# Kernel tuning notes

Measured on AMD Instinct MI355X. Metric: run time of the kernel, lower is better.

Reference implementation:

```python
import jax, jax.numpy as jnp
import numpy as np

N = 20000
E_RAND = 320000
NEG_SLOPE = 0.2


def setup_inputs() -> dict:
    key = jax.random.key(0)
    ks = jax.random.split(key, 10)
    x = jax.random.normal(ks[0], (N, 768), dtype=jnp.float32)
    src = jax.random.randint(ks[1], (E_RAND,), 0, N)
    dst = jax.random.randint(ks[2], (E_RAND,), 0, N)
    loop = jnp.arange(N)
    edge_index = jnp.stack([jnp.concatenate([src, loop]),
                            jnp.concatenate([dst, loop])])  # [2, 340000]
    s = 1.0 / np.sqrt(768.0)
    W1 = jax.random.normal(ks[3], (768, 768), dtype=jnp.float32) * s
    a_src1 = jax.random.normal(ks[4], (8, 96), dtype=jnp.float32) * 0.1
    a_dst1 = jax.random.normal(ks[5], (8, 96), dtype=jnp.float32) * 0.1
    b1 = jnp.zeros((768,), dtype=jnp.float32)
    W2 = jax.random.normal(ks[6], (768, 768), dtype=jnp.float32) * s
    a_src2 = jax.random.normal(ks[7], (1, 768), dtype=jnp.float32) * 0.1
    a_dst2 = jax.random.normal(ks[8], (1, 768), dtype=jnp.float32) * 0.1
    b2 = jnp.zeros((768,), dtype=jnp.float32)
    return {"x": x, "edge_index": edge_index, "W1": W1, "a_src1": a_src1,
            "a_dst1": a_dst1, "b1": b1, "W2": W2, "a_src2": a_src2,
            "a_dst2": a_dst2, "b2": b2}


def gat_layer(x, W, a_src, a_dst, bias, src, dst, heads, out_c, concat):
    n = x.shape[0]
    h = (x @ W).reshape(n, heads, out_c)                      # [N,H,C]
    al_s = jnp.einsum('nhc,hc->nh', h, a_src)                 # [N,H]
    al_d = jnp.einsum('nhc,hc->nh', h, a_dst)
    e = jax.nn.leaky_relu(al_s[src] + al_d[dst], NEG_SLOPE)   # [E,H]
    m = jax.ops.segment_max(e, dst, num_segments=n)           # segment softmax
    ex = jnp.exp(e - m[dst])
    z = jax.ops.segment_sum(ex, dst, num_segments=n)
    alpha = ex / (z[dst] + 1e-16)                             # [E,H]
    msg = h[src] * alpha[:, :, None]                          # [E,H,C]
    out = jax.ops.segment_sum(msg, dst, num_segments=n)       # [N,H,C]
    out = out.reshape(n, heads * out_c) if concat else out.mean(axis=1)
    return out + bias


def reference(x, edge_index, W1, a_src1, a_dst1, b1, W2, a_src2, a_dst2, b2):
    src, dst = edge_index[0], edge_index[1]
    h = gat_layer(x, W1, a_src1, a_dst1, b1, src, dst, heads=8, out_c=96, concat=True)
    h = jax.nn.elu(h)
    out = gat_layer(h, W2, a_src2, a_dst2, b2, src, dst, heads=1, out_c=768, concat=False)
    return out
```

## Files before the change

### kernel.cpp

```cpp
#include <hip/hip_runtime.h>
#include <cstdint>
#include <cstddef>

typedef _Float16 f16;
typedef _Float16 f16x4 __attribute__((ext_vector_type(4)));
typedef _Float16 f16x8 __attribute__((ext_vector_type(8)));
typedef float f32x4 __attribute__((ext_vector_type(4)));

#define LRELU_SLOPE 0.2f

#define GLL16(g, l)                                                          \
  __builtin_amdgcn_global_load_lds(                                          \
      (const __attribute__((address_space(1))) void*)(g),                    \
      (__attribute__((address_space(3))) void*)(l), 16, 0, 0)

__global__ __launch_bounds__(256) void k_prep_xh(const float* __restrict__ x,
                                                 f16* __restrict__ xh,
                                                 int nvalid, int npad) {
  int total = npad * 192;
  for (int idx = blockIdx.x * blockDim.x + threadIdx.x; idx < total;
       idx += gridDim.x * blockDim.x) {
    int row = idx / 192;
    f16x4 o;
    if (row < nvalid) {
      const float4 v = *(const float4*)(x + (size_t)idx * 4);
      o[0] = (f16)v.x; o[1] = (f16)v.y; o[2] = (f16)v.z; o[3] = (f16)v.w;
    } else {
      o[0] = (f16)0.f; o[1] = (f16)0.f; o[2] = (f16)0.f; o[3] = (f16)0.f;
    }
    *(f16x4*)(xh + (size_t)idx * 4) = o;
  }
}

__global__ __launch_bounds__(256) void k_transpose_w2(const float* __restrict__ W1,
                                                      const float* __restrict__ W2,
                                                      f16* __restrict__ Wt1,
                                                      f16* __restrict__ Wt2) {
  const float* W = blockIdx.z ? W2 : W1;
  f16* Wt = blockIdx.z ? Wt2 : Wt1;
  __shared__ float tile[32][33];
  int bn = blockIdx.x * 32;
  int bk = blockIdx.y * 32;
  int tx = threadIdx.x & 31, ty = threadIdx.x >> 5;
  #pragma unroll
  for (int r = ty; r < 32; r += 8)
    tile[r][tx] = W[(size_t)(bk + r) * 768 + bn + tx];
  __syncthreads();
  #pragma unroll
  for (int r = ty; r < 32; r += 8)
    Wt[(size_t)(bn + r) * 768 + bk + tx] = (f16)tile[tx][r];
}

__global__ void k_hist(const int* __restrict__ dst, int E, int* __restrict__ counts) {
  for (int e = blockIdx.x * blockDim.x + threadIdx.x; e < E;
       e += gridDim.x * blockDim.x) atomicAdd(&counts[dst[e]], 1);
}

__global__ __launch_bounds__(1024) void k_scan_block(const int* __restrict__ counts,
                                                     int* __restrict__ starts,
                                                     int* __restrict__ cursor, int n) {
  const int t = threadIdx.x;
  const int nthr = 1024;
  const int chunk = (n + nthr - 1) / nthr;
  const int base = t * chunk;
  int tsum = 0;
  for (int i = 0; i < chunk; i++) {
    int idx = base + i;
    if (idx < n) tsum += counts[idx];
  }
  int lane = t & 63, wv = t >> 6;
  int s = tsum;
  #pragma unroll
  for (int off = 1; off < 64; off <<= 1) {
    int tmp = __shfl_up(s, off);
    if (lane >= off) s += tmp;
  }
  __shared__ int wsum[16];
  if (lane == 63) wsum[wv] = s;
  __syncthreads();
  int woff = 0;
  for (int w = 0; w < wv; w++) woff += wsum[w];
  int run = woff + s - tsum;
  for (int i = 0; i < chunk; i++) {
    int idx = base + i;
    if (idx < n) {
      starts[idx] = run;
      cursor[idx] = run;
      run += counts[idx];
    }
  }
  if (t == nthr - 1) starts[n] = run;
}

__global__ void k_fill(const int* __restrict__ src, const int* __restrict__ dst, int E,
                       int* __restrict__ cursor, int* __restrict__ src_sorted) {
  for (int e = blockIdx.x * blockDim.x + threadIdx.x; e < E;
       e += gridDim.x * blockDim.x) {
    int slot = atomicAdd(&cursor[dst[e]], 1);
    src_sorted[slot] = src[e];
  }
}

__global__ __launch_bounds__(256) void k_gemm_f16(const f16* __restrict__ A,
                                                  const f16* __restrict__ Bt,
                                                  f16* __restrict__ C, int Mvalid) {
  __shared__ __align__(16) f16 As[2][8192];
  __shared__ __align__(16) f16 Bs[2][8192];
  const int K = 768;
  const int tid = threadIdx.x;

  const int nwg = gridDim.x;
  const int orig = blockIdx.x;
  const int q = nwg >> 3, r = nwg & 7;
  const int xcd = orig & 7;
  const int wgid = (xcd < r ? xcd * (q + 1) : r * (q + 1) + (xcd - r) * q) + (orig >> 3);
  const int bm = (wgid / 6) * 128;
  const int bn = (wgid - (wgid / 6) * 6) * 128;

  const int lane = tid & 63;
  const int wave = tid >> 6;
  const int wr = (wave >> 1) * 64;
  const int wc = (wave & 1) * 64;

  size_t goffA[4], goffB[4];
  #pragma unroll
  for (int p = 0; p < 4; p++) {
    const int cell = p * 256 + tid;
    const int row = cell >> 3;
    const int cl = (cell & 7) ^ (row & 7);
    goffA[p] = (size_t)(bm + row) * K + cl * 8;
    goffB[p] = (size_t)(bn + row) * K + cl * 8;
  }

  f32x4 acc[4][4];
  const f32x4 vzero = {0.f, 0.f, 0.f, 0.f};
  #pragma unroll
  for (int i = 0; i < 4; i++)
    #pragma unroll
    for (int j = 0; j < 4; j++) acc[i][j] = vzero;

  const int fr = lane & 15;
  const int fq = lane >> 4;

  #define STAGE(buf, k0)                                                      \
    do {                                                                      \
      _Pragma("unroll")                                                       \
      for (int p = 0; p < 4; p++) {                                           \
        GLL16(A + goffA[p] + (k0), &As[buf][p * 2048 + wave * 512]);          \
        GLL16(Bt + goffB[p] + (k0), &Bs[buf][p * 2048 + wave * 512]);         \
      }                                                                       \
    } while (0)

  STAGE(0, 0);
  asm volatile("s_waitcnt vmcnt(0)" ::: "memory");
  __builtin_amdgcn_s_barrier();

  const int NT = K / 64;
  int cur = 0;
  for (int t = 0; t < NT; t++) {
    if (t + 1 < NT) STAGE(cur ^ 1, (t + 1) * 64);
    #pragma unroll
    for (int ks = 0; ks < 2; ks++) {
      f16x8 af[4], bf[4];
      #pragma unroll
      for (int i = 0; i < 4; i++) {
        const int rr = wr + i * 16 + fr;
        const int phys = (ks * 4 + fq) ^ (rr & 7);
        af[i] = *(const f16x8*)(&As[cur][rr * 64 + phys * 8]);
      }
      #pragma unroll
      for (int j = 0; j < 4; j++) {
        const int rr = wc + j * 16 + fr;
        const int phys = (ks * 4 + fq) ^ (rr & 7);
        bf[j] = *(const f16x8*)(&Bs[cur][rr * 64 + phys * 8]);
      }
      #pragma unroll
      for (int i = 0; i < 4; i++)
        #pragma unroll
        for (int j = 0; j < 4; j++)
          acc[i][j] = __builtin_amdgcn_mfma_f32_16x16x32_f16(af[i], bf[j], acc[i][j], 0, 0, 0);
    }
    asm volatile("s_waitcnt vmcnt(0)" ::: "memory");
    __builtin_amdgcn_s_barrier();
    cur ^= 1;
  }
  #undef STAGE

  #pragma unroll
  for (int i = 0; i < 4; i++) {
    #pragma unroll
    for (int j = 0; j < 4; j++) {
      const int col = bn + wc + j * 16 + fr;
      #pragma unroll
      for (int rg = 0; rg < 4; rg++) {
        const int row = bm + wr + i * 16 + fq * 4 + rg;
        if (row < Mvalid) C[(size_t)row * 768 + col] = (f16)acc[i][j][rg];
      }
    }
  }
}

template <int H>
__global__ __launch_bounds__(256) void k_al(const f16* __restrict__ h,
                                            const float* __restrict__ a_src,
                                            const float* __restrict__ a_dst,
                                            float* __restrict__ als,
                                            float* __restrict__ ald, int N) {
  int node = blockIdx.x * 4 + (threadIdx.x >> 6);
  int lane = threadIdx.x & 63;
  if (node >= N) return;
  const f16x4* hp = (const f16x4*)(h + (size_t)node * 768 + lane * 12);
  float ss = 0.f, sd = 0.f;
  int cbase = lane * 12;
  #pragma unroll
  for (int q = 0; q < 3; q++) {
    f16x4 hv = hp[q];
    #pragma unroll
    for (int j = 0; j < 4; j++) {
      int c = cbase + q * 4 + j;
      float v = (float)hv[j];
      ss += v * a_src[c];
      sd += v * a_dst[c];
    }
  }
  const int red = (H == 8) ? 8 : 64;
  #pragma unroll
  for (int off = 1; off < red; off <<= 1) {
    ss += __shfl_xor(ss, off);
    sd += __shfl_xor(sd, off);
  }
  if (H == 8) {
    if ((lane & 7) == 0) {
      als[(size_t)node * 8 + (lane >> 3)] = ss;
      ald[(size_t)node * 8 + (lane >> 3)] = sd;
    }
  } else {
    if (lane == 0) { als[node] = ss; ald[node] = sd; }
  }
}

template <int H, bool FINAL>
__global__ __launch_bounds__(192) void k_aggregate(
    const f16* __restrict__ h, const float* __restrict__ als,
    const float* __restrict__ ald, const int* __restrict__ starts,
    const int* __restrict__ src_sorted, const float* __restrict__ bias,
    void* __restrict__ outv, int nvalid) {
  const int n = blockIdx.x;
  const int t = threadIdx.x;
  if (n >= nvalid) return;
  __shared__ float s_ex[256 * H];
  __shared__ int s_src[256];
  __shared__ float s_zp[3][H];
  const int start = starts[n];
  const int deg = starts[n + 1] - start;
  const int lane = t & 63, wv = t >> 6;
  const int hA = (H == 8) ? (t & 7) : 0;
  const int myh = (H == 8) ? (t / 24) : 0;
  const float ald_A = ald[(size_t)n * H + hA];

  float zpart = 0.f;
  float4 acc = {0.f, 0.f, 0.f, 0.f};

  for (int cb = 0; cb < deg; cb += 256) {
    const int cnt = min(256, deg - cb);
    for (int idx = t; idx < cnt * H; idx += 192) {
      const int e = (H == 8) ? (idx >> 3) : idx;
      const int s = src_sorted[start + cb + e];
      if (H == 1 || (idx & 7) == 0) s_src[e] = s;
      float v = als[(size_t)s * H + hA] + ald_A;
      v = v > 0.f ? v : LRELU_SLOPE * v;
      const float ex = __expf(v);
      s_ex[idx] = ex;
      zpart += ex;
    }
    __syncthreads();
    for (int e = 0; e < cnt; e++) {
      const f16x4 hv = *(const f16x4*)(h + (size_t)s_src[e] * 768 + 4 * t);
      const float a = s_ex[e * H + myh];
      acc.x += a * (float)hv[0];
      acc.y += a * (float)hv[1];
      acc.z += a * (float)hv[2];
      acc.w += a * (float)hv[3];
    }
    __syncthreads();
  }

  if (H == 8) {
    #pragma unroll
    for (int off = 8; off < 64; off <<= 1) zpart += __shfl_xor(zpart, off);
    if (lane < 8) s_zp[wv][lane] = zpart;
  } else {
    #pragma unroll
    for (int off = 1; off < 64; off <<= 1) zpart += __shfl_xor(zpart, off);
    if (lane == 0) s_zp[wv][0] = zpart;
  }
  __syncthreads();
  const float z = s_zp[0][myh] + s_zp[1][myh] + s_zp[2][myh];
  const float inv = 1.f / (z + 1e-16f);

  const float4 bv = *(const float4*)(bias + 4 * t);
  float v0 = acc.x * inv + bv.x;
  float v1 = acc.y * inv + bv.y;
  float v2 = acc.z * inv + bv.z;
  float v3 = acc.w * inv + bv.w;
  if (!FINAL) {
    v0 = v0 > 0.f ? v0 : expm1f(v0);
    v1 = v1 > 0.f ? v1 : expm1f(v1);
    v2 = v2 > 0.f ? v2 : expm1f(v2);
    v3 = v3 > 0.f ? v3 : expm1f(v3);
    f16x4 o;
    o[0] = (f16)v0; o[1] = (f16)v1; o[2] = (f16)v2; o[3] = (f16)v3;
    *(f16x4*)((f16*)outv + (size_t)n * 768 + 4 * t) = o;
  } else {
    float4 o = {v0, v1, v2, v3};
    *(float4*)((float*)outv + (size_t)n * 768 + 4 * t) = o;
  }
}

extern "C" void kernel_launch(void* const* d_in, const int* in_sizes, int n_in,
                              void* d_out, int out_size, void* d_ws, size_t ws_size,
                              hipStream_t stream) {
  const float* x   = (const float*)d_in[0];
  const int*   ei  = (const int*)d_in[1];
  const float* W1  = (const float*)d_in[2];
  const float* as1 = (const float*)d_in[3];
  const float* ad1 = (const float*)d_in[4];
  const float* b1  = (const float*)d_in[5];
  const float* W2  = (const float*)d_in[6];
  const float* as2 = (const float*)d_in[7];
  const float* ad2 = (const float*)d_in[8];
  const float* b2  = (const float*)d_in[9];

  const int N = in_sizes[0] / 768;
  const int E = in_sizes[1] / 2;
  const int Mpad = (N + 127) & ~127;
  const int* srcp = ei;
  const int* dstp = ei + E;

  char* p = (char*)d_ws;
  auto alloc = [&](size_t b) { char* r = p; p += (b + 255) & ~(size_t)255; return r; };
  f16*   bufX   = (f16*)alloc((size_t)Mpad * 768 * sizeof(f16));
  f16*   bufH   = (f16*)alloc((size_t)Mpad * 768 * sizeof(f16));
  f16*   Wt1    = (f16*)alloc((size_t)768 * 768 * sizeof(f16));
  f16*   Wt2    = (f16*)alloc((size_t)768 * 768 * sizeof(f16));
  float* als1   = (float*)alloc((size_t)N * 8 * sizeof(float));
  float* ald1   = (float*)alloc((size_t)N * 8 * sizeof(float));
  float* als2   = (float*)alloc((size_t)N * sizeof(float));
  float* ald2   = (float*)alloc((size_t)N * sizeof(float));
  int*   counts = (int*)alloc((size_t)N * sizeof(int));
  int*   starts = (int*)alloc(((size_t)N + 1) * sizeof(int));
  int*   cursor = (int*)alloc((size_t)N * sizeof(int));
  int*   srcs   = (int*)alloc((size_t)E * sizeof(int));

  hipMemsetAsync(counts, 0, (size_t)N * sizeof(int), stream);
  k_hist<<<dim3(512), dim3(256), 0, stream>>>(dstp, E, counts);
  k_scan_block<<<dim3(1), dim3(1024), 0, stream>>>(counts, starts, cursor, N);
  k_fill<<<dim3(512), dim3(256), 0, stream>>>(srcp, dstp, E, cursor, srcs);

  k_prep_xh<<<dim3(1024), dim3(256), 0, stream>>>(x, bufX, N, Mpad);
  k_transpose_w2<<<dim3(24, 24, 2), dim3(256), 0, stream>>>(W1, W2, Wt1, Wt2);

  const int nwg = (Mpad / 128) * 6;

  k_gemm_f16<<<dim3(nwg), dim3(256), 0, stream>>>(bufX, Wt1, bufH, N);
  k_al<8><<<dim3((N + 3) / 4), dim3(256), 0, stream>>>(bufH, as1, ad1, als1, ald1, N);
  k_aggregate<8, false><<<dim3(N), dim3(192), 0, stream>>>(bufH, als1, ald1, starts, srcs, b1, bufX, N);

  k_gemm_f16<<<dim3(nwg), dim3(256), 0, stream>>>(bufX, Wt2, bufH, N);
  k_al<1><<<dim3((N + 3) / 4), dim3(256), 0, stream>>>(bufH, as2, ad2, als2, ald2, N);
  k_aggregate<1, true><<<dim3(N), dim3(192), 0, stream>>>(bufH, als2, ald2, starts, srcs, b2, d_out, N);
}
```

Baseline: 320.1 us.

## Load GEMM A fragments directly to registers and split layer-1 aggregation launch

The GEMM no longer stages the A tile through LDS. Each wave loads its A fragments straight from global memory into registers and prefetches the next k-step one iteration ahead, which halves LDS use and sets a 3-blocks-per-CU launch bound. The goal is to cut LDS traffic and footprint so more workgroups fit per CU, at the cost of more registers and uncoalesced direct global loads of A. Separately, the layer-1 aggregation is split into two launches over halves of the nodes, which adds a launch without an obvious speed reason.

```diff
diff --git a/kernel.cpp b/kernel.cpp
--- a/kernel.cpp
+++ b/kernel.cpp
@@ -101,10 +101,9 @@
   }
 }
 
-__global__ __launch_bounds__(256) void k_gemm_f16(const f16* __restrict__ A,
-                                                  const f16* __restrict__ Bt,
-                                                  f16* __restrict__ C, int Mvalid) {
-  __shared__ __align__(16) f16 As[2][8192];
+__global__ __launch_bounds__(256, 3) void k_gemm_f16(const f16* __restrict__ A,
+                                                     const f16* __restrict__ Bt,
+                                                     f16* __restrict__ C, int Mvalid) {
   __shared__ __align__(16) f16 Bs[2][8192];
   const int K = 768;
   const int tid = threadIdx.x;
@@ -121,16 +120,22 @@
   const int wave = tid >> 6;
   const int wr = (wave >> 1) * 64;
   const int wc = (wave & 1) * 64;
-
-  size_t goffA[4], goffB[4];
+  const int fr = lane & 15;
+  const int fq = lane >> 4;
+
+  size_t goffB[4];
   #pragma unroll
   for (int p = 0; p < 4; p++) {
     const int cell = p * 256 + tid;
     const int row = cell >> 3;
     const int cl = (cell & 7) ^ (row & 7);
-    goffA[p] = (size_t)(bm + row) * K + cl * 8;
     goffB[p] = (size_t)(bn + row) * K + cl * 8;
   }
+
+  const f16* arow[4];
+  #pragma unroll
+  for (int i = 0; i < 4; i++)
+    arow[i] = A + (size_t)(bm + wr + i * 16 + fr) * K + fq * 8;
 
   f32x4 acc[4][4];
   const f32x4 vzero = {0.f, 0.f, 0.f, 0.f};
@@ -139,35 +144,37 @@
     #pragma unroll
     for (int j = 0; j < 4; j++) acc[i][j] = vzero;
 
-  const int fr = lane & 15;
-  const int fq = lane >> 4;
-
-  #define STAGE(buf, k0)                                                      \
+  #define STAGEB(buf, k0)                                                     \
     do {                                                                      \
       _Pragma("unroll")                                                       \
-      for (int p = 0; p < 4; p++) {                                           \
-        GLL16(A + goffA[p] + (k0), &As[buf][p * 2048 + wave * 512]);          \
+      for (int p = 0; p < 4; p++)                                             \
         GLL16(Bt + goffB[p] + (k0), &Bs[buf][p * 2048 + wave * 512]);         \
-      }                                                                       \
     } while (0)
 
-  STAGE(0, 0);
+  const int NT = K / 64;
+  STAGEB(0, 0);
+  f16x8 aC[2][4], aN[2][4];
+  #pragma unroll
+  for (int ks = 0; ks < 2; ks++)
+    #pragma unroll
+    for (int i = 0; i < 4; i++)
+      aC[ks][i] = *(const f16x8*)(arow[i] + ks * 32);
   asm volatile("s_waitcnt vmcnt(0)" ::: "memory");
   __builtin_amdgcn_s_barrier();
 
-  const int NT = K / 64;
-  int cur = 0;
+  #pragma unroll 2
   for (int t = 0; t < NT; t++) {
-    if (t + 1 < NT) STAGE(cur ^ 1, (t + 1) * 64);
+    const int cur = t & 1;
+    const int kn = (t + 1 < NT) ? (t + 1) * 64 : t * 64;
+    STAGEB(cur ^ 1, kn);
+    #pragma unroll
+    for (int ks = 0; ks < 2; ks++)
+      #pragma unroll
+      for (int i = 0; i < 4; i++)
+        aN[ks][i] = *(const f16x8*)(arow[i] + kn + ks * 32);
     #pragma unroll
     for (int ks = 0; ks < 2; ks++) {
-      f16x8 af[4], bf[4];
-      #pragma unroll
-      for (int i = 0; i < 4; i++) {
-        const int rr = wr + i * 16 + fr;
-        const int phys = (ks * 4 + fq) ^ (rr & 7);
-        af[i] = *(const f16x8*)(&As[cur][rr * 64 + phys * 8]);
-      }
+      f16x8 bf[4];
       #pragma unroll
       for (int j = 0; j < 4; j++) {
         const int rr = wc + j * 16 + fr;
@@ -178,13 +185,17 @@
       for (int i = 0; i < 4; i++)
         #pragma unroll
         for (int j = 0; j < 4; j++)
-          acc[i][j] = __builtin_amdgcn_mfma_f32_16x16x32_f16(af[i], bf[j], acc[i][j], 0, 0, 0);
+          acc[i][j] = __builtin_amdgcn_mfma_f32_16x16x32_f16(aC[ks][i], bf[j], acc[i][j], 0, 0, 0);
     }
     asm volatile("s_waitcnt vmcnt(0)" ::: "memory");
     __builtin_amdgcn_s_barrier();
-    cur ^= 1;
-  }
-  #undef STAGE
+    #pragma unroll
+    for (int ks = 0; ks < 2; ks++)
+      #pragma unroll
+      for (int i = 0; i < 4; i++)
+        aC[ks][i] = aN[ks][i];
+  }
+  #undef STAGEB
 
   #pragma unroll
   for (int i = 0; i < 4; i++) {
@@ -244,8 +255,8 @@
     const f16* __restrict__ h, const float* __restrict__ als,
     const float* __restrict__ ald, const int* __restrict__ starts,
     const int* __restrict__ src_sorted, const float* __restrict__ bias,
-    void* __restrict__ outv, int nvalid) {
-  const int n = blockIdx.x;
+    void* __restrict__ outv, int nvalid, int nbase) {
+  const int n = nbase + blockIdx.x;
   const int t = threadIdx.x;
   if (n >= nvalid) return;
   __shared__ float s_ex[256 * H];
@@ -361,12 +372,18 @@
   k_transpose_w2<<<dim3(24, 24, 2), dim3(256), 0, stream>>>(W1, W2, Wt1, Wt2);
 
   const int nwg = (Mpad / 128) * 6;
+  const int nh1 = (N + 1) / 2;
+  const int nh2 = N - nh1;
 
   k_gemm_f16<<<dim3(nwg), dim3(256), 0, stream>>>(bufX, Wt1, bufH, N);
   k_al<8><<<dim3((N + 3) / 4), dim3(256), 0, stream>>>(bufH, as1, ad1, als1, ald1, N);
-  k_aggregate<8, false><<<dim3(N), dim3(192), 0, stream>>>(bufH, als1, ald1, starts, srcs, b1, bufX, N);
+  k_aggregate<8, false><<<dim3(nh1), dim3(192), 0, stream>>>(
+      bufH, als1, ald1, starts, srcs, b1, bufX, N, 0);
+  k_aggregate<8, false><<<dim3(nh2), dim3(192), 0, stream>>>(
+      bufH, als1, ald1, starts, srcs, b1, bufX, N, nh1);
 
   k_gemm_f16<<<dim3(nwg), dim3(256), 0, stream>>>(bufX, Wt2, bufH, N);
   k_al<1><<<dim3((N + 3) / 4), dim3(256), 0, stream>>>(bufH, as2, ad2, als2, ald2, N);
-  k_aggregate<1, true><<<dim3(N), dim3(192), 0, stream>>>(bufH, als2, ald2, starts, srcs, b2, d_out, N);
-}
+  k_aggregate<1, true><<<dim3(N), dim3(192), 0, stream>>>(
+      bufH, als2, ald2, starts, srcs, b2, d_out, N, 0);
+}
```

Result: slower. 385.9 us (+20.5%).
